# Performance work log

Measured on AMD Instinct MI355X. Metric: run time of the kernel, lower is better.

The kernel has to match this reference:

```python
import jax, jax.numpy as jnp
import numpy as np

B, DZ, DIM, T = 4096, 512, 63, 120  # batch, dim_z, pose dim, input_len
H = 2 * DZ  # LSTMCell hidden size


def setup_inputs() -> dict:
    key = jax.random.key(0)
    ks = jax.random.split(key, 9)
    s = 0.02
    w = lambda k, shp: jax.random.normal(k, shp, dtype=jnp.float32) * s
    z = lambda n: jnp.zeros((n,), jnp.float32)
    return {
        "x": jax.random.normal(ks[0], (B, DZ), dtype=jnp.float32),
        "W_lin": w(ks[1], (DZ, DZ)), "b_lin": z(DZ),
        "W_p1": w(ks[2], (DZ, DZ)), "b_p1": z(DZ),
        "W_p2": w(ks[3], (DIM, DZ)), "b_p2": z(DIM),
        "W_ih": w(ks[4], (4 * H, DZ + DIM)), "b_ih": z(4 * H),
        "W_hh": w(ks[5], (4 * H, H)), "b_hh": z(4 * H),
        "W_1": w(ks[6], (DZ, H)), "b_1": z(DZ),
        "W_2": w(ks[7], (DIM, DZ)), "b_2": z(DIM),
        "input_len": T,
    }


def reference(x, W_lin, b_lin, W_p1, b_p1, W_p2, b_p2,
              W_ih, b_ih, W_hh, b_hh, W_1, b_1, W_2, b_2, input_len):
    relu = jax.nn.relu
    x = relu(x @ W_lin.T + b_lin)                      # [B, DZ]
    pose = relu(x @ W_p1.T + b_p1) @ W_p2.T + b_p2     # [B, DIM]
    hdim = W_hh.shape[1]
    h0 = jnp.zeros((x.shape[0], hdim), x.dtype)

    def step(carry, _):
        h, c, pose = carry
        inp = jnp.concatenate([x, pose], axis=1)       # [B, DZ+DIM]
        gates = inp @ W_ih.T + b_ih + h @ W_hh.T + b_hh  # [B, 4H]
        i, f, g, o = jnp.split(gates, 4, axis=1)       # torch LSTMCell gate order
        c = jax.nn.sigmoid(f) * c + jax.nn.sigmoid(i) * jnp.tanh(g)
        h = jax.nn.sigmoid(o) * jnp.tanh(c)
        pose = relu(h @ W_1.T + b_1) @ W_2.T + b_2     # residual=False
        return (h, c, pose), pose

    _, outs = jax.lax.scan(step, (h0, h0, pose), None, length=input_len)
    return jnp.transpose(outs, (1, 0, 2))              # [B, T, DIM]
```

## Files before the change

### kernel.cpp

```cpp
#include <hip/hip_runtime.h>
#include <hip/hip_bf16.h>

#define DEV __device__ __forceinline__

typedef _Float16 f16;
typedef _Float16 f16x8 __attribute__((ext_vector_type(8)));
typedef _Float16 f16x4 __attribute__((ext_vector_type(4)));
typedef float    f32x4 __attribute__((ext_vector_type(4)));

constexpr int Bsz = 4096;
constexpr int DZ  = 512;
constexpr int DIM = 63;
constexpr int T   = 120;
constexpr int H   = 1024;
constexpr int G4  = 4096;
constexpr int KC  = 1088;

DEV void gload16(f16* lds_p, const f16* g) {
  __builtin_amdgcn_global_load_lds(
      (const __attribute__((address_space(1))) unsigned int*)g,
      (__attribute__((address_space(3))) unsigned int*)lds_p, 16, 0, 0);
}

DEV float sigf(float x) { return 1.f / (1.f + __expf(-x)); }
DEV float tanh_fast(float x) { float e = __expf(2.f * x); return (e - 1.f) / (e + 1.f); }

enum { EPI_RELU_F16 = 0, EPI_F16 = 1, EPI_GATESX = 2, EPI_POSE = 4 };

struct GArgs {
  const f16* A;  int ldA;
  const f16* Bm; int ldB;
  int K;
  const float* bias;
  f16* O; int ldO;
  f16* inp;
  float* outp; int t;
};

template <int BM, int BN, int WM, int WN, int EPI>
__global__ __launch_bounds__((BM / WM) * (BN / WN) * 64)
void gemm_k(GArgs p) {
  constexpr int WN_CNT = BN / WN;
  constexpr int NW = (BM / WM) * WN_CNT;
  constexpr int NT = NW * 64;
  constexpr int MF = WM / 16, NF = WN / 16;
  constexpr int AIT = BM * 8 / NT, BIT = BN * 8 / NT;
  constexpr int RPI = NT / 8;

  __shared__ __align__(16) f16 sA[BM * 64];
  __shared__ __align__(16) f16 sB[BN * 64];

  const int tid = threadIdx.x, lane = tid & 63;
  const int wv = tid >> 6, wm = wv / WN_CNT, wn = wv % WN_CNT;
  const int bm = blockIdx.x, bn = blockIdx.y;

  f32x4 acc[MF][NF] = {};

  const int sr = tid >> 3;
  const int sc = (tid & 7) * 8;
  const f16* gA = p.A + (size_t)(bm * BM + sr) * p.ldA + sc;
  const f16* gB = p.Bm + (size_t)(bn * BN + sr) * p.ldB + sc;
  f16* lA = sA + tid * 8;
  f16* lB = sB + tid * 8;

  for (int k0 = 0; k0 < p.K; k0 += 64) {
#pragma unroll
    for (int it = 0; it < AIT; ++it)
      gload16(lA + it * NT * 8, gA + (size_t)it * RPI * p.ldA + k0);
#pragma unroll
    for (int it = 0; it < BIT; ++it)
      gload16(lB + it * NT * 8, gB + (size_t)it * RPI * p.ldB + k0);
    __syncthreads();
#pragma unroll
    for (int kk = 0; kk < 2; ++kk) {
      f16x8 af[MF], bf[NF];
#pragma unroll
      for (int i = 0; i < MF; ++i)
        af[i] = *(const f16x8*)(sA + (wm * WM + i * 16 + (lane & 15)) * 64 + kk * 32 + (lane >> 4) * 8);
#pragma unroll
      for (int j = 0; j < NF; ++j)
        bf[j] = *(const f16x8*)(sB + (wn * WN + j * 16 + (lane & 15)) * 64 + kk * 32 + (lane >> 4) * 8);
#pragma unroll
      for (int i = 0; i < MF; ++i)
#pragma unroll
        for (int j = 0; j < NF; ++j)
          acc[i][j] = __builtin_amdgcn_mfma_f32_16x16x32_f16(af[i], bf[j], acc[i][j], 0, 0, 0);
    }
    __syncthreads();
  }

  const int r0 = bm * BM + wm * WM;
  const int c0 = bn * BN + wn * WN;

  if constexpr (EPI == EPI_POSE) {
#pragma unroll
    for (int i = 0; i < MF; ++i)
#pragma unroll
      for (int j = 0; j < NF; ++j)
#pragma unroll
        for (int r = 0; r < 4; ++r) {
          const int row = r0 + i * 16 + ((lane >> 4) << 2) + r;
          const int col = c0 + j * 16 + (lane & 15);
          float v = acc[i][j][r] + p.bias[col];
          p.inp[(size_t)row * KC + H + col] = (f16)v;
          if (col < DIM)
            p.outp[(size_t)row * (T * DIM) + (size_t)p.t * DIM + col] = v;
        }
  } else {
#pragma unroll
    for (int i = 0; i < MF; ++i)
#pragma unroll
      for (int j = 0; j < NF; ++j)
#pragma unroll
        for (int r = 0; r < 4; ++r) {
          const int row = r0 + i * 16 + ((lane >> 4) << 2) + r;
          const int col = c0 + j * 16 + (lane & 15);
          float v = acc[i][j][r] + p.bias[col];
          if constexpr (EPI == EPI_RELU_F16) v = fmaxf(v, 0.f);
          if constexpr (EPI == EPI_GATESX)
            p.O[(size_t)row * G4 + ((size_t)(col & 1023) << 2) + (col >> 10)] = (f16)v;
          else
            p.O[(size_t)row * p.ldO + col] = (f16)v;
        }
  }
}


#define WAITV(N) asm volatile("s_waitcnt vmcnt(" #N ")" ::: "memory")
#define BARRIER()                          \
  {                                        \
    asm volatile("" ::: "memory");         \
    __builtin_amdgcn_s_barrier();          \
    asm volatile("" ::: "memory");         \
  }

#define RD_A(SLOT, MH, DST)                                                         \
  _Pragma("unroll") for (int fi = 0; fi < 4; ++fi)                                  \
  _Pragma("unroll") for (int kk = 0; kk < 2; ++kk)                                  \
      DST[fi * 2 + kk] = *(const f16x8*)(lds + (SLOT) * 32768 +                     \
          (mb + ((MH) * 4 + fi) * 16) * 64 + ((kk * 32 + ck0) ^ swf));

#define RD_B(SLOT, NH, DST)                                                         \
  _Pragma("unroll") for (int fj = 0; fj < 2; ++fj)                                  \
  _Pragma("unroll") for (int kk = 0; kk < 2; ++kk)                                  \
      DST[fj * 2 + kk] = *(const f16x8*)(lds + (SLOT) * 32768 + 16384 +             \
          (nb + ((NH) * 2 + fj) * 16) * 64 + ((kk * 32 + ck0) ^ swf));

#define MFMA8(MH, NH, A_, B_)                                                       \
  __builtin_amdgcn_s_setprio(1);                                                    \
  _Pragma("unroll") for (int kk = 0; kk < 2; ++kk)                                  \
  _Pragma("unroll") for (int fi = 0; fi < 4; ++fi)                                  \
  _Pragma("unroll") for (int fj = 0; fj < 2; ++fj)                                  \
      acc[(MH) * 4 + fi][(NH) * 2 + fj] = __builtin_amdgcn_mfma_f32_16x16x32_f16(   \
          A_[fi * 2 + kk], B_[fj * 2 + kk], acc[(MH) * 4 + fi][(NH) * 2 + fj], 0, 0, 0); \
  __builtin_amdgcn_s_setprio(0);

#define ST_A(D, IT, TILE) \
  gload16(ldsA + (D) * 32768 + (IT) * 4096, gA + (size_t)(64 * (IT)) * KC + (TILE) * 64)
#define ST_B(D, IT, TILE) \
  gload16(ldsB + (D) * 32768 + (IT) * 4096, gB + (size_t)(16 * (IT)) * KC + (TILE) * 64)

__global__ __launch_bounds__(512, 2)
void lstm_gates_8ph(const f16* __restrict__ A, const f16* __restrict__ Bw,
                    const f16* __restrict__ gx, float* __restrict__ c32,
                    f16* __restrict__ inp) {
  __shared__ __align__(16) f16 lds[65536];

  const int tid = threadIdx.x, lane = tid & 63;
  const int wv = tid >> 6, wm = wv >> 2, wn = wv & 3;
  const int bm = blockIdx.x, bn = blockIdx.y;

  const int rr = tid >> 3;
  const int c0 = (tid & 7) * 8;
  const int swst = (rr & 7) << 3;
  const int cs = c0 ^ swst;
  const f16* gA = A + (size_t)(bm * 256 + rr) * KC + cs;
  const int grow0 = (tid >> 7) * 1024 + bn * 64 + ((tid >> 3) & 15);
  const f16* gB = Bw + (size_t)grow0 * KC + cs;
  f16* ldsA = lds + tid * 8;
  f16* ldsB = lds + 16384 + tid * 8;

  const int ck0 = (lane >> 4) * 8;
  const int swf = (lane & 7) << 3;
  const int mb = wm * 128 + (lane & 15);
  const int nb = wn * 64 + (lane & 15);

  f32x4 acc[8][4] = {};
  f16x8 afr[8], bfr0[4], bfr1[4];

  ST_A(0, 0, 0); ST_A(0, 2, 0);
  ST_B(0, 0, 0); ST_B(0, 1, 0);
  ST_B(0, 2, 0); ST_B(0, 3, 0);
  ST_A(0, 1, 0); ST_A(0, 3, 0);

  for (int kt = 0; kt < 16; ++kt) {
    const int s = kt & 1, d = s ^ 1, nt = kt + 1;
    WAITV(2); BARRIER();
    RD_A(s, 0, afr); RD_B(s, 0, bfr0);
    ST_A(d, 0, nt); ST_A(d, 2, nt);
    MFMA8(0, 0, afr, bfr0);
    BARRIER();
    RD_B(s, 1, bfr1);
    ST_B(d, 0, nt); ST_B(d, 1, nt);
    ST_B(d, 2, nt); ST_B(d, 3, nt);
    MFMA8(0, 1, afr, bfr1);
    WAITV(6); BARRIER();
    RD_A(s, 1, afr);
    ST_A(d, 1, nt); ST_A(d, 3, nt);
    MFMA8(1, 1, afr, bfr1);
    BARRIER();
    MFMA8(1, 0, afr, bfr0);
  }

  WAITV(2); BARRIER();
  RD_A(0, 0, afr); RD_B(0, 0, bfr0);
  MFMA8(0, 0, afr, bfr0);
  RD_B(0, 1, bfr1);
  MFMA8(0, 1, afr, bfr1);
  WAITV(0); BARRIER();
  RD_A(0, 1, afr);
  MFMA8(1, 1, afr, bfr1);
  MFMA8(1, 0, afr, bfr0);

  const int jg = (bn * 4 + wn) * 16 + (lane & 15);
  const int r0 = bm * 256 + wm * 128;
#pragma unroll
  for (int i = 0; i < 8; ++i) {
#pragma unroll
    for (int r = 0; r < 4; ++r) {
      const int row = r0 + i * 16 + ((lane >> 4) << 2) + r;
      f16x4 g4v = *(const f16x4*)(gx + (size_t)row * G4 + jg * 4);
      float ig = acc[i][0][r] + (float)g4v[0];
      float fg = acc[i][1][r] + (float)g4v[1];
      float gg = acc[i][2][r] + (float)g4v[2];
      float og = acc[i][3][r] + (float)g4v[3];
      float c = c32[(size_t)row * H + jg];
      c = sigf(fg) * c + sigf(ig) * tanh_fast(gg);
      float h = sigf(og) * tanh_fast(c);
      c32[(size_t)row * H + jg] = c;
      inp[(size_t)row * KC + jg] = (f16)h;
    }
  }
}

__global__ void k_cvt(const float* s, f16* d, int n) {
  for (int i = blockIdx.x * blockDim.x + threadIdx.x; i < n; i += gridDim.x * blockDim.x)
    d[i] = (f16)s[i];
}
__global__ void k_pad_rows(const float* s, f16* d, int rows, int n) {
  for (int i = blockIdx.x * blockDim.x + threadIdx.x; i < n; i += gridDim.x * blockDim.x) {
    int r = i >> 9;
    d[i] = (r < rows) ? (f16)s[i] : (f16)0.f;
  }
}
__global__ void k_pack_wihx(const float* W, f16* d) {
  for (int i = blockIdx.x * blockDim.x + threadIdx.x; i < G4 * DZ; i += gridDim.x * blockDim.x) {
    int n = i >> 9, k = i & 511;
    d[i] = (f16)W[n * 575 + k];
  }
}
__global__ void k_pack_wcat(const float* Wih, const float* Whh, f16* d) {
  for (int i = blockIdx.x * blockDim.x + threadIdx.x; i < G4 * KC; i += gridDim.x * blockDim.x) {
    int n = i / KC, k = i - n * KC;
    float v = (k < H) ? Whh[n * H + k] : ((k < H + DIM) ? Wih[n * 575 + DZ + (k - H)] : 0.f);
    d[i] = (f16)v;
  }
}
__global__ void k_bias(const float* bih, const float* bhh, float* bsum,
                       const float* bp2, float* bp2p, const float* b2, float* b2p) {
  int i = blockIdx.x * blockDim.x + threadIdx.x;
  if (i < G4) bsum[i] = bih[i] + bhh[i];
  if (i < 64) {
    bp2p[i] = (i < DIM) ? bp2[i] : 0.f;
    b2p[i]  = (i < DIM) ? b2[i]  : 0.f;
  }
}
__global__ void k_init(float* c32, f16* inp) {
  for (int i = blockIdx.x * blockDim.x + threadIdx.x; i < Bsz * H; i += gridDim.x * blockDim.x) {
    c32[i] = 0.f;
    inp[(size_t)(i >> 10) * KC + (i & 1023)] = (f16)0.f;
  }
}

extern "C" void kernel_launch(void* const* d_in, const int* in_sizes, int n_in,
                              void* d_out, int out_size, void* d_ws, size_t ws_size,
                              hipStream_t stream) {
  const float* x_in = (const float*)d_in[0];
  const float* Wlin = (const float*)d_in[1];
  const float* blin = (const float*)d_in[2];
  const float* Wp1  = (const float*)d_in[3];
  const float* bp1  = (const float*)d_in[4];
  const float* Wp2  = (const float*)d_in[5];
  const float* bp2  = (const float*)d_in[6];
  const float* Wih  = (const float*)d_in[7];
  const float* bih  = (const float*)d_in[8];
  const float* Whh  = (const float*)d_in[9];
  const float* bhh  = (const float*)d_in[10];
  const float* W1   = (const float*)d_in[11];
  const float* b1   = (const float*)d_in[12];
  const float* W2   = (const float*)d_in[13];
  const float* b2   = (const float*)d_in[14];
  float* out = (float*)d_out;

  char* w = (char*)d_ws;
  auto alloc = [&](size_t bytes) { char* r = w; w += (bytes + 255) & ~(size_t)255; return r; };
  f16*   inpA   = (f16*)alloc((size_t)Bsz * KC * 2);
  f16*   inpB   = (f16*)alloc((size_t)Bsz * KC * 2);
  float* c32    = (float*)alloc((size_t)Bsz * H * 4);
  f16*   gx16   = (f16*)alloc((size_t)Bsz * G4 * 2);
  f16*   wcat   = (f16*)alloc((size_t)G4 * KC * 2);
  f16*   wihx   = (f16*)alloc((size_t)G4 * DZ * 2);
  f16*   wlin16 = (f16*)alloc((size_t)DZ * DZ * 2);
  f16*   wp1_16 = (f16*)alloc((size_t)DZ * DZ * 2);
  f16*   wp2p   = (f16*)alloc((size_t)64 * DZ * 2);
  f16*   w1_16  = (f16*)alloc((size_t)DZ * H * 2);
  f16*   w2p    = (f16*)alloc((size_t)64 * DZ * 2);
  f16*   xin16  = (f16*)alloc((size_t)Bsz * DZ * 2);
  f16*   x16    = (f16*)alloc((size_t)Bsz * DZ * 2);
  f16*   t16    = (f16*)alloc((size_t)Bsz * DZ * 2);
  float* bsum   = (float*)alloc((size_t)G4 * 4);
  float* bp2p_  = (float*)alloc(64 * 4);
  float* b2p    = (float*)alloc(64 * 4);

  dim3 blk(256);
  auto g1 = [](int n) { int b = (n + 255) / 256; return dim3(b > 2048 ? 2048 : b); };

  k_cvt<<<g1(Bsz * DZ), blk, 0, stream>>>(x_in, xin16, Bsz * DZ);
  k_cvt<<<g1(DZ * DZ), blk, 0, stream>>>(Wlin, wlin16, DZ * DZ);
  k_cvt<<<g1(DZ * DZ), blk, 0, stream>>>(Wp1, wp1_16, DZ * DZ);
  k_cvt<<<g1(DZ * H), blk, 0, stream>>>(W1, w1_16, DZ * H);
  k_pad_rows<<<g1(64 * DZ), blk, 0, stream>>>(Wp2, wp2p, DIM, 64 * DZ);
  k_pad_rows<<<g1(64 * DZ), blk, 0, stream>>>(W2, w2p, DIM, 64 * DZ);
  k_pack_wihx<<<g1(G4 * DZ), blk, 0, stream>>>(Wih, wihx);
  k_pack_wcat<<<g1(G4 * KC), blk, 0, stream>>>(Wih, Whh, wcat);
  k_bias<<<16, blk, 0, stream>>>(bih, bhh, bsum, bp2, bp2p_, b2, b2p);
  k_init<<<g1(Bsz * H), blk, 0, stream>>>(c32, inpA);

  GArgs a{};
  a.A = xin16; a.ldA = DZ; a.Bm = wlin16; a.ldB = DZ; a.K = DZ;
  a.bias = blin; a.O = x16; a.ldO = DZ;
  gemm_k<64, 128, 32, 64, EPI_RELU_F16><<<dim3(Bsz / 64, 4), 256, 0, stream>>>(a);
  a.A = x16; a.Bm = wp1_16; a.bias = bp1; a.O = t16;
  gemm_k<64, 128, 32, 64, EPI_RELU_F16><<<dim3(Bsz / 64, 4), 256, 0, stream>>>(a);
  GArgs a3{};
  a3.A = t16; a3.ldA = DZ; a3.Bm = wp2p; a3.ldB = DZ; a3.K = DZ;
  a3.bias = bp2p_; a3.O = inpA + H; a3.ldO = KC;
  gemm_k<64, 64, 32, 32, EPI_F16><<<dim3(Bsz / 64, 1), 256, 0, stream>>>(a3);
  GArgs a4{};
  a4.A = x16; a4.ldA = DZ; a4.Bm = wihx; a4.ldB = DZ; a4.K = DZ;
  a4.bias = bsum; a4.O = gx16;
  gemm_k<128, 128, 32, 128, EPI_GATESX><<<dim3(Bsz / 128, G4 / 128), 256, 0, stream>>>(a4);

  for (int t = 0; t < T; ++t) {
    f16* cur = (t & 1) ? inpB : inpA;
    f16* nxt = (t & 1) ? inpA : inpB;
    lstm_gates_8ph<<<dim3(16, 16), 512, 0, stream>>>(cur, wcat, gx16, c32, nxt);
    GArgs s2{};
    s2.A = nxt; s2.ldA = KC; s2.Bm = w1_16; s2.ldB = H; s2.K = H;
    s2.bias = b1; s2.O = t16; s2.ldO = DZ;
    gemm_k<64, 128, 32, 64, EPI_RELU_F16><<<dim3(Bsz / 64, 4), 256, 0, stream>>>(s2);
    GArgs s3{};
    s3.A = t16; s3.ldA = DZ; s3.Bm = w2p; s3.ldB = DZ; s3.K = DZ;
    s3.bias = b2p; s3.inp = nxt; s3.outp = out; s3.t = t;
    gemm_k<32, 64, 16, 32, EPI_POSE><<<dim3(Bsz / 32, 1), 256, 0, stream>>>(s3);
  }
}
```

Before: 8.516 ms.

## Fuse post-LSTM MLP GEMMs into one kernel and remap gate blocks per XCD

Each step's two post-LSTM GEMMs (h→relu(W1) and →W2 pose) are merged into one kernel. Each block computes 32 rows across the full 512 hidden width, keeps the intermediate in LDS, and writes pose to the next input buffer and the output. This removes a launch and the global round-trip of the t16 intermediate per step. The trade-off is only 128 blocks and heavier redundant W1 reads per block. Separately, the gates kernel now uses a 1D grid whose block index is remapped so neighbouring N-tiles land on the same XCD, aiming for better L2 reuse of weights.

```diff
diff --git a/kernel.cpp b/kernel.cpp
--- a/kernel.cpp
+++ b/kernel.cpp
@@ -168,7 +168,10 @@
 
   const int tid = threadIdx.x, lane = tid & 63;
   const int wv = tid >> 6, wm = wv >> 2, wn = wv & 3;
-  const int bm = blockIdx.x, bn = blockIdx.y;
+  const int id = blockIdx.x;
+  const int xcd = id & 7, idx = id >> 3;
+  const int bn = xcd * 2 + (idx & 1);
+  const int bm = idx >> 1;
 
   const int rr = tid >> 3;
   const int c0 = (tid & 7) * 8;
@@ -240,6 +243,107 @@
       c32[(size_t)row * H + jg] = c;
       inp[(size_t)row * KC + jg] = (f16)h;
     }
+  }
+}
+
+__global__ __launch_bounds__(512, 1)
+void fused_s23(const f16* __restrict__ inpr, const f16* __restrict__ W1,
+               const float* __restrict__ b1, const f16* __restrict__ W2p,
+               const float* __restrict__ b2pp, f16* __restrict__ inpw,
+               float* __restrict__ outp, int t) {
+  __shared__ __align__(16) f16 lds[69632];
+
+  const int tid = threadIdx.x, lane = tid & 63, wv = tid >> 6;
+  const int bm = blockIdx.x;
+
+  const int rrA = (tid & 255) >> 3;
+  const int rrB = tid >> 3;
+  const int c0 = (tid & 7) * 8;
+  const f16* gA = inpr + (size_t)(bm * 32 + rrA) * KC + (c0 ^ ((rrA & 7) << 3));
+  const f16* gB = W1 + (size_t)rrB * H + (c0 ^ ((rrB & 7) << 3));
+
+  const int ck0 = (lane >> 4) * 8;
+  const int swf = (lane & 7) << 3;
+
+  auto STAGE = [&](int d, int k0) {
+    f16* Lb = lds + d * 34816;
+    if (wv < 4) gload16(Lb + (tid & 255) * 8, gA + k0);
+#pragma unroll
+    for (int it = 0; it < 8; ++it)
+      gload16(Lb + 2048 + it * 4096 + tid * 8, gB + (size_t)(it * 64) * H + k0);
+  };
+
+  f32x4 acc[2][4] = {};
+
+  STAGE(0, 0);
+  for (int kt = 0; kt < 16; ++kt) {
+    const int s = kt & 1;
+    if (kt < 15) {
+      STAGE(s ^ 1, (kt + 1) * 64);
+      if (wv < 4) { WAITV(9); } else { WAITV(8); }
+    } else {
+      WAITV(0);
+    }
+    BARRIER();
+    const f16* Ls = lds + s * 34816;
+#pragma unroll
+    for (int kk = 0; kk < 2; ++kk) {
+      f16x8 af[2], bf[4];
+#pragma unroll
+      for (int i = 0; i < 2; ++i)
+        af[i] = *(const f16x8*)(Ls + (i * 16 + (lane & 15)) * 64 + ((kk * 32 + ck0) ^ swf));
+#pragma unroll
+      for (int j = 0; j < 4; ++j)
+        bf[j] = *(const f16x8*)(Ls + 2048 + (wv * 64 + j * 16 + (lane & 15)) * 64 + ((kk * 32 + ck0) ^ swf));
+#pragma unroll
+      for (int i = 0; i < 2; ++i)
+#pragma unroll
+        for (int j = 0; j < 4; ++j)
+          acc[i][j] = __builtin_amdgcn_mfma_f32_16x16x32_f16(af[i], bf[j], acc[i][j], 0, 0, 0);
+    }
+    BARRIER();
+  }
+
+  float b1v[4];
+#pragma unroll
+  for (int j = 0; j < 4; ++j) b1v[j] = b1[wv * 64 + j * 16 + (lane & 15)];
+#pragma unroll
+  for (int i = 0; i < 2; ++i)
+#pragma unroll
+    for (int j = 0; j < 4; ++j)
+#pragma unroll
+      for (int r = 0; r < 4; ++r) {
+        const int row = i * 16 + ((lane >> 4) << 2) + r;
+        const int col = wv * 64 + j * 16 + (lane & 15);
+        float v = fmaxf(acc[i][j][r] + b1v[j], 0.f);
+        lds[row * 512 + (col ^ ((row & 7) << 3))] = (f16)v;
+      }
+#pragma unroll
+  for (int it = 0; it < 8; ++it) {
+    const int q = it * 512 + tid, rw = q >> 6, cc = q & 63;
+    gload16(lds + 34816 + q * 8, W2p + (size_t)rw * 512 + ((cc * 8) ^ ((rw & 7) << 3)));
+  }
+  __syncthreads();
+
+  const int wm2 = wv & 1, wn2 = wv >> 1;
+  const int ra = (wm2 * 16 + (lane & 15)) * 512;
+  const int rb = 34816 + (wn2 * 16 + (lane & 15)) * 512;
+  f32x4 pacc = {};
+#pragma unroll
+  for (int ks = 0; ks < 16; ++ks) {
+    f16x8 a = *(const f16x8*)(lds + ra + ((ks * 32 + ck0) ^ swf));
+    f16x8 b = *(const f16x8*)(lds + rb + ((ks * 32 + ck0) ^ swf));
+    pacc = __builtin_amdgcn_mfma_f32_16x16x32_f16(a, b, pacc, 0, 0, 0);
+  }
+  const int pcol = wn2 * 16 + (lane & 15);
+  const float pb = b2pp[pcol];
+#pragma unroll
+  for (int r = 0; r < 4; ++r) {
+    const int row = bm * 32 + wm2 * 16 + ((lane >> 4) << 2) + r;
+    float v = pacc[r] + pb;
+    inpw[(size_t)row * KC + H + pcol] = (f16)v;
+    if (pcol < DIM)
+      outp[(size_t)row * (T * DIM) + (size_t)t * DIM + pcol] = v;
   }
 }
 
@@ -354,14 +458,7 @@
   for (int t = 0; t < T; ++t) {
     f16* cur = (t & 1) ? inpB : inpA;
     f16* nxt = (t & 1) ? inpA : inpB;
-    lstm_gates_8ph<<<dim3(16, 16), 512, 0, stream>>>(cur, wcat, gx16, c32, nxt);
-    GArgs s2{};
-    s2.A = nxt; s2.ldA = KC; s2.Bm = w1_16; s2.ldB = H; s2.K = H;
-    s2.bias = b1; s2.O = t16; s2.ldO = DZ;
-    gemm_k<64, 128, 32, 64, EPI_RELU_F16><<<dim3(Bsz / 64, 4), 256, 0, stream>>>(s2);
-    GArgs s3{};
-    s3.A = t16; s3.ldA = DZ; s3.Bm = w2p; s3.ldB = DZ; s3.K = DZ;
-    s3.bias = b2p; s3.inp = nxt; s3.outp = out; s3.t = t;
-    gemm_k<32, 64, 16, 32, EPI_POSE><<<dim3(Bsz / 32, 1), 256, 0, stream>>>(s3);
-  }
-}
+    lstm_gates_8ph<<<dim3(256), 512, 0, stream>>>(cur, wcat, gx16, c32, nxt);
+    fused_s23<<<dim3(128), 512, 0, stream>>>(nxt, w1_16, b1, w2p, b2p, nxt, out, t);
+  }
+}
```

Measured after the change: 7.714 ms. 9.4% less time.
